# Kernel optimization log

Hardware: AMD Instinct MI355X
Metric: run time of the kernel (lower is better)

Reference implementation:

```python
import jax, jax.numpy as jnp
import numpy as np

B, S, D, H = 2, 2048, 1024, 16
DK = D // H
ROPE_BASE = 10000.0


def setup_inputs() -> dict:
    key = jax.random.key(0)
    ks = jax.random.split(key, 6)
    x = jax.random.normal(ks[0], (B, S, D), dtype=jnp.float32)
    # causal mask, broadcastable to [B,H,S,S]; masked_fill where mask==0
    mask = jnp.tril(jnp.ones((S, S), dtype=bool))[None, None]
    position_ids = jnp.tile(jnp.arange(S, dtype=jnp.int32)[None, :], (B, 1))
    sc = 1.0 / np.sqrt(D)
    Wq = jax.random.normal(ks[1], (D, D), dtype=jnp.float32) * sc
    Wk = jax.random.normal(ks[2], (D, D), dtype=jnp.float32) * sc
    Wv = jax.random.normal(ks[3], (D, D), dtype=jnp.float32) * sc
    Wo = jax.random.normal(ks[4], (D, D), dtype=jnp.float32) * sc
    bo = jnp.zeros((D,), dtype=jnp.float32)
    return {"x": x, "mask": mask, "position_ids": position_ids,
            "Wq": Wq, "Wk": Wk, "Wv": Wv, "Wo": Wo, "bo": bo}


def _rotate_half(t):
    t1, t2 = t[..., : t.shape[-1] // 2], t[..., t.shape[-1] // 2:]
    return jnp.concatenate((-t2, t1), axis=-1)


def reference(x, mask, position_ids, Wq, Wk, Wv, Wo, bo):
    b, s, d = x.shape
    h, dk = H, DK
    scale = 1.0 / np.sqrt(dk)

    def proj(W):  # torch Linear: x @ W.T -> [b,h,s,dk]
        return (x @ W.T).reshape(b, s, h, dk).transpose(0, 2, 1, 3)

    Q, K, V = proj(Wq), proj(Wk), proj(Wv)

    # rotary tables (computed in fp32, matching RotaryEmbedding)
    inv_freq = 1.0 / (ROPE_BASE ** (jnp.arange(0, dk, 2, dtype=jnp.float32) / dk))
    t = jnp.arange(s, dtype=jnp.float32)
    freqs = jnp.outer(t, inv_freq)            # [s, dk/2]
    emb = jnp.concatenate((freqs, freqs), -1) # [s, dk]
    cos = jnp.cos(emb)[position_ids][:, None]  # [b,1,s,dk]
    sin = jnp.sin(emb)[position_ids][:, None]
    Q = Q * cos + _rotate_half(Q) * sin
    K = K * cos + _rotate_half(K) * sin

    scores = jnp.einsum('bhqd,bhkd->bhqk', Q, K) * scale
    scores = jnp.where(mask, scores, jnp.float32(-1e9))
    attn = jax.nn.softmax(scores, axis=-1)  # dropout is identity in eval
    out = jnp.einsum('bhqk,bhkd->bhqd', attn, V)
    out = out.transpose(0, 2, 1, 3).reshape(b, s, d)
    return out @ Wo.T + bo
```

## Files before the change

### kernel.cpp

```cpp
#include <hip/hip_runtime.h>
#include <hip/hip_bf16.h>
#include <cstdint>

#define BB 2
#define SS 2048
#define DD 1024
#define HH 16
#define DK 64
#define MROWS (BB*SS)
#define NQKV  (3*DD)

typedef __bf16 bf16x8 __attribute__((ext_vector_type(8)));
typedef float  f32x4  __attribute__((ext_vector_type(4)));
typedef float  f32x16 __attribute__((ext_vector_type(16)));
typedef unsigned u32x2 __attribute__((ext_vector_type(2)));

static __device__ __forceinline__ unsigned short f2bf(float f) {
    __bf16 h = (__bf16)f;
    return __builtin_bit_cast(unsigned short, h);
}
static __device__ __forceinline__ float bf2f(unsigned short u) {
    return (float)__builtin_bit_cast(__bf16, u);
}

#define GLOAD16(gsrc, ldst) \
    __builtin_amdgcn_global_load_lds((const __attribute__((address_space(1))) void*)(gsrc), \
                                     (__attribute__((address_space(3))) void*)(ldst), 16, 0, 0)

static __device__ __forceinline__ void pl32_swap(unsigned &x, unsigned &y) {
#if __has_builtin(__builtin_amdgcn_permlane32_swap)
    u32x2 r = __builtin_amdgcn_permlane32_swap(x, y, false, false);
    x = r[0]; y = r[1];
#else
    asm volatile("v_permlane32_swap_b32 %0, %1" : "+v"(x), "+v"(y));
#endif
}
static __device__ __forceinline__ float swap_half(float v, bool hi) {
    unsigned x = __builtin_bit_cast(unsigned, v), y = x;
    pl32_swap(x, y);
    return __builtin_bit_cast(float, hi ? x : y);
}
template<int BASE> static __device__ __forceinline__ bf16x8 cvt_chunk(const f32x16 &p) {
    unsigned x0, y0, x1, y1;
    asm("v_cvt_pk_bf16_f32 %0, %1, %2" : "=v"(x0) : "v"(p[BASE+0]), "v"(p[BASE+1]));
    asm("v_cvt_pk_bf16_f32 %0, %1, %2" : "=v"(y0) : "v"(p[BASE+4]), "v"(p[BASE+5]));
    asm("v_cvt_pk_bf16_f32 %0, %1, %2" : "=v"(x1) : "v"(p[BASE+2]), "v"(p[BASE+3]));
    asm("v_cvt_pk_bf16_f32 %0, %1, %2" : "=v"(y1) : "v"(p[BASE+6]), "v"(p[BASE+7]));
    pl32_swap(x0, y0);
    pl32_swap(x1, y1);
    union { unsigned u[4]; bf16x8 v; } r;
    r.u[0] = x0; r.u[1] = x1; r.u[2] = y0; r.u[3] = y1;
    return r.v;
}

__global__ void cast_all(const float* __restrict__ x,  const float* __restrict__ wq,
                         const float* __restrict__ wk, const float* __restrict__ wv,
                         const float* __restrict__ wo,
                         unsigned short* __restrict__ xb, unsigned short* __restrict__ wqkv,
                         unsigned short* __restrict__ wob)
{
    const int NX = MROWS * DD;
    const int NW = DD * DD;
    const int total = (NX + 4 * NW) / 8;
    for (int i = blockIdx.x * blockDim.x + threadIdx.x; i < total; i += gridDim.x * blockDim.x) {
        int base = i * 8;
        const float* src; unsigned short* dst; int off;
        if      (base < NX)          { src = x;  dst = xb;          off = base; }
        else if (base < NX + NW)     { src = wq; dst = wqkv;        off = base - NX; }
        else if (base < NX + 2*NW)   { src = wk; dst = wqkv + NW;   off = base - NX - NW; }
        else if (base < NX + 3*NW)   { src = wv; dst = wqkv + 2*NW; off = base - NX - 2*NW; }
        else                         { src = wo; dst = wob;         off = base - NX - 3*NW; }
        float4 a = *(const float4*)(src + off);
        float4 b = *(const float4*)(src + off + 4);
        union { unsigned short s[8]; uint4 v; } u;
        u.s[0] = f2bf(a.x); u.s[1] = f2bf(a.y); u.s[2] = f2bf(a.z); u.s[3] = f2bf(a.w);
        u.s[4] = f2bf(b.x); u.s[5] = f2bf(b.y); u.s[6] = f2bf(b.z); u.s[7] = f2bf(b.w);
        *(uint4*)(dst + off) = u.v;
    }
}

__global__ void rope_table(float* __restrict__ tabc, float* __restrict__ tabs)
{
    int i = blockIdx.x * blockDim.x + threadIdx.x;
    int s = i >> 5, d = i & 31;
    float inv = exp2f(-(float)d * (13.287712379549449f / 32.f));
    float ang = (float)s * inv;
    tabc[i] = cosf(ang);
    tabs[i] = sinf(ang);
}

__global__ __launch_bounds__(256) void gemm_qkv(
    const unsigned short* __restrict__ A, const unsigned short* __restrict__ Bm,
    const int* __restrict__ pids,
    const float* __restrict__ tabc, const float* __restrict__ tabs,
    unsigned short* __restrict__ Qb, unsigned short* __restrict__ Kb,
    unsigned short* __restrict__ Vr)
{
    __shared__ __align__(16) unsigned short sA[128 * 64];
    __shared__ __align__(16) unsigned short sB[128 * 64];
    const int tid = threadIdx.x;
    const int w = tid >> 6, l = tid & 63;
    const int wm = w >> 1, wn = w & 1;
    const int lr = l & 15, lg = l >> 4;
    const int swz = (blockIdx.x & 7) * 96 + (blockIdx.x >> 3);
    const int bx = swz % 24, by = swz / 24;
    const int mBase = by * 128, nBase = bx * 128;
    const int srow = tid >> 3;
    const int skof = (tid & 7) * 8;

    f32x4 acc[4][4] = {};

    for (int kt = 0; kt < DD; kt += 64) {
        __syncthreads();
        #pragma unroll
        for (int i = 0; i < 4; ++i) {
            const unsigned short* srcA = A + (size_t)(mBase + i*32 + srow) * DD + kt + skof;
            GLOAD16(srcA, &sA[i*2048 + w*512]);
            const unsigned short* srcB = Bm + (size_t)(nBase + i*32 + srow) * DD + kt + skof;
            GLOAD16(srcB, &sB[i*2048 + w*512]);
        }
        __syncthreads();
        #pragma unroll
        for (int kk = 0; kk < 2; ++kk) {
            bf16x8 af[4], bfv[4];
            #pragma unroll
            for (int mi = 0; mi < 4; ++mi)
                af[mi] = *(const bf16x8*)&sA[(wm*64 + mi*16 + lr)*64 + kk*32 + lg*8];
            #pragma unroll
            for (int ni = 0; ni < 4; ++ni)
                bfv[ni] = *(const bf16x8*)&sB[(wn*64 + ni*16 + lr)*64 + kk*32 + lg*8];
            #pragma unroll
            for (int mi = 0; mi < 4; ++mi)
                #pragma unroll
                for (int ni = 0; ni < 4; ++ni)
                    acc[mi][ni] = __builtin_amdgcn_mfma_f32_16x16x32_bf16(af[mi], bfv[ni], acc[mi][ni], 0, 0, 0);
        }
    }

    if (bx < 16) {
        const bool isQ = bx < 8;
        unsigned short* dst = isQ ? Qb : Kb;
        const float qsc = isQ ? 0.1803368801111244f : 1.0f;
        const int colbase = (bx & 7)*128 + wn*64;
        #pragma unroll
        for (int mi = 0; mi < 4; ++mi) {
            #pragma unroll
            for (int j = 0; j < 4; ++j) {
                int row = mBase + wm*64 + mi*16 + lg*4 + j;
                int pos = pids[row];
                #pragma unroll
                for (int ni = 0; ni < 2; ++ni) {
                    int d = ni*16 + lr;
                    float cc = tabc[pos*32 + d];
                    float sn = tabs[pos*32 + d];
                    float a  = acc[mi][ni][j];
                    float bb = acc[mi][ni+2][j];
                    dst[(size_t)row * DD + colbase + d]      = f2bf((a*cc - bb*sn) * qsc);
                    dst[(size_t)row * DD + colbase + d + 32] = f2bf((bb*cc + a*sn) * qsc);
                }
            }
        }
    } else {
        const int colbase = (bx - 16)*128 + wn*64;
        #pragma unroll
        for (int mi = 0; mi < 4; ++mi) {
            #pragma unroll
            for (int j = 0; j < 4; ++j) {
                int row = mBase + wm*64 + mi*16 + lg*4 + j;
                #pragma unroll
                for (int ni = 0; ni < 4; ++ni)
                    Vr[(size_t)row * DD + colbase + ni*16 + lr] = f2bf(acc[mi][ni][j]);
            }
        }
    }
}

__global__ __launch_bounds__(256) void gemm_bt(
    const unsigned short* __restrict__ A, const unsigned short* __restrict__ Bm,
    float* __restrict__ Cout, const float* __restrict__ bias,
    int M, int N, int K)
{
    __shared__ __align__(16) unsigned short sA[2][128 * 64];
    __shared__ __align__(16) unsigned short sB[2][128 * 64];
    const int tid = threadIdx.x;
    const int w = tid >> 6, l = tid & 63;
    const int wm = w >> 1, wn = w & 1;
    const int lr = l & 15, lg = l >> 4;
    const int nwg = gridDim.x;
    const int cpx = nwg >> 3;
    const int swz = (blockIdx.x & 7) * cpx + (blockIdx.x >> 3);
    const int nbx = N >> 7;
    const int bx = swz % nbx, by = swz / nbx;
    const int mBase = by * 128, nBase = bx * 128;
    const int srow = tid >> 3;
    const int skof = (tid & 7) * 8;

    f32x4 acc[4][4] = {};

    #pragma unroll
    for (int i = 0; i < 4; ++i) {
        GLOAD16(A  + (size_t)(mBase + i*32 + srow) * K + skof, &sA[0][i*2048 + w*512]);
        GLOAD16(Bm + (size_t)(nBase + i*32 + srow) * K + skof, &sB[0][i*2048 + w*512]);
    }
    int cur = 0;

    for (int kt = 0; kt < K; kt += 64) {
        __syncthreads();
        if (kt + 64 < K) {
            #pragma unroll
            for (int i = 0; i < 4; ++i) {
                GLOAD16(A  + (size_t)(mBase + i*32 + srow) * K + kt + 64 + skof, &sA[cur^1][i*2048 + w*512]);
                GLOAD16(Bm + (size_t)(nBase + i*32 + srow) * K + kt + 64 + skof, &sB[cur^1][i*2048 + w*512]);
            }
        }
        #pragma unroll
        for (int kk = 0; kk < 2; ++kk) {
            bf16x8 af[4], bfv[4];
            #pragma unroll
            for (int mi = 0; mi < 4; ++mi)
                af[mi] = *(const bf16x8*)&sA[cur][(wm*64 + mi*16 + lr)*64 + kk*32 + lg*8];
            #pragma unroll
            for (int ni = 0; ni < 4; ++ni)
                bfv[ni] = *(const bf16x8*)&sB[cur][(wn*64 + ni*16 + lr)*64 + kk*32 + lg*8];
            #pragma unroll
            for (int mi = 0; mi < 4; ++mi)
                #pragma unroll
                for (int ni = 0; ni < 4; ++ni)
                    acc[mi][ni] = __builtin_amdgcn_mfma_f32_16x16x32_bf16(af[mi], bfv[ni], acc[mi][ni], 0, 0, 0);
        }
        cur ^= 1;
    }
    #pragma unroll
    for (int mi = 0; mi < 4; ++mi) {
        #pragma unroll
        for (int j = 0; j < 4; ++j) {
            int row = mBase + wm*64 + mi*16 + lg*4 + j;
            #pragma unroll
            for (int ni = 0; ni < 4; ++ni) {
                int col = nBase + wn*64 + ni*16 + lr;
                Cout[(size_t)row * N + col] = acc[mi][ni][j] + bias[col];
            }
        }
    }
}

__global__ __launch_bounds__(256) void v_transpose(
    const unsigned short* __restrict__ Vr, unsigned short* __restrict__ Vt)
{
    __shared__ __align__(16) unsigned short sT[64 * 64];
    const int bh = blockIdx.y;
    const int st = blockIdx.x;
    const int b = bh >> 4, h = bh & 15;
    const int tid = threadIdx.x;
    #pragma unroll
    for (int i = 0; i < 2; ++i) {
        int c = tid + i*256;
        int s = c >> 3, cb = c & 7;
        const unsigned short* src = Vr + (size_t)(b*SS + st*64 + s) * DD + h*64 + cb*8;
        uint4 v = *(const uint4*)src;
        *(uint4*)&sT[s*64 + ((cb ^ (s >> 3)) * 8)] = v;
    }
    __syncthreads();
    #pragma unroll
    for (int i = 0; i < 2; ++i) {
        int c = tid + i*256;
        int d = c >> 3, sb = c & 7;
        union { unsigned short u[8]; uint4 v; } o;
        #pragma unroll
        for (int e = 0; e < 8; ++e) {
            int s = sb*8 + e;
            o.u[e] = sT[s*64 + (((d >> 3) ^ (s >> 3)) * 8) + (d & 7)];
        }
        *(uint4*)(Vt + (size_t)(bh*64 + d) * SS + st*64 + sb*8) = o.v;
    }
}

__global__ __launch_bounds__(256, 2) void attn_fwd(
    const unsigned short* __restrict__ Qb,
    const unsigned short* __restrict__ Kb,
    const unsigned short* __restrict__ Vt,
    unsigned short* __restrict__ Ob)
{
    __shared__ __align__(16) unsigned short sK[2][64 * 64];
    __shared__ __align__(16) unsigned short sV[2][64 * 64];
    const int tid = threadIdx.x;
    const int w = tid >> 6, l = tid & 63;
    const int lq = l & 31;
    const int hi5 = l >> 5;
    const bool hb = hi5 != 0;

    const int xcd  = blockIdx.x & 7;
    const int c    = blockIdx.x >> 3;
    const int gsel = c & 3;
    const int t    = c >> 2;
    const int qt   = (t < 8) ? t : 23 - t;
    const int bh   = xcd * 4 + gsel;
    const int b = bh >> 4, h = bh & 15;

    const int srow = tid >> 3;
    const int skof = (tid & 7) * 8;
    const int sksw = skof ^ ((srow & 7) * 8);
    const int sw   = (lq & 7) * 8;
    const float THR = 12.0f;

    const unsigned kR0 = (unsigned)((b*SS + srow) * DD + h*64 + sksw);
    const unsigned kR1 = kR0 + (unsigned)(32 * DD);
    const unsigned vR0 = (unsigned)((bh*64 + srow) * SS + sksw);
    const unsigned vR1 = vR0 + (unsigned)(32 * SS);

    bf16x8 qf[4];
    {
        const unsigned short* qp = Qb + (size_t)(b*SS + qt*128 + w*32 + lq) * DD + h*64 + hi5*8;
        #pragma unroll
        for (int dkc = 0; dkc < 4; ++dkc)
            qf[dkc] = *(const bf16x8*)(qp + dkc*16);
    }
    const int q_lane = qt*128 + w*32 + lq;
    const int wbase  = qt*128 + w*32;
    const int total  = 2*qt + 2;

    f32x16 o0 = {}, o1 = {};
    float mrow = -3.0e38f, lsum = 0.f;
    int cur = 0;

    GLOAD16(Kb + kR0, &sK[0][w*512]);
    GLOAD16(Kb + kR1, &sK[0][2048 + w*512]);
    GLOAD16(Vt + vR0, &sV[0][w*512]);
    GLOAD16(Vt + vR1, &sV[0][2048 + w*512]);

    for (int kt = 0; kt < total; ++kt) {
        __syncthreads();
        if (kt + 1 < total) {
            unsigned ko = (unsigned)(kt + 1) << 16;
            unsigned vo = (unsigned)(kt + 1) << 6;
            GLOAD16(Kb + kR0 + ko, &sK[cur^1][w*512]);
            GLOAD16(Kb + kR1 + ko, &sK[cur^1][2048 + w*512]);
            GLOAD16(Vt + vR0 + vo, &sV[cur^1][w*512]);
            GLOAD16(Vt + vR1 + vo, &sV[cur^1][2048 + w*512]);
        }

        f32x16 p0 = {}, p1 = {};
        __builtin_amdgcn_s_setprio(1);
        #pragma unroll
        for (int dkc = 0; dkc < 4; ++dkc) {
            bf16x8 k0 = *(const bf16x8*)&sK[cur][lq*64 + ((dkc*16 + hi5*8) ^ sw)];
            p0 = __builtin_amdgcn_mfma_f32_32x32x16_bf16(k0, qf[dkc], p0, 0, 0, 0);
        }
        #pragma unroll
        for (int dkc = 0; dkc < 4; ++dkc) {
            bf16x8 k1 = *(const bf16x8*)&sK[cur][(32 + lq)*64 + ((dkc*16 + hi5*8) ^ sw)];
            p1 = __builtin_amdgcn_mfma_f32_32x32x16_bf16(k1, qf[dkc], p1, 0, 0, 0);
        }
        __builtin_amdgcn_s_setprio(0);

        if (kt*64 + 63 > wbase) {
            const int kb0 = kt*64 + 4*hi5;
            #pragma unroll
            for (int r = 0; r < 16; ++r) {
                const int cr = (r & 3) + 8*(r >> 2);
                if (kb0 + cr > q_lane)      p0[r] = -1e30f;
                if (kb0 + 32 + cr > q_lane) p1[r] = -1e30f;
            }
        }

        float tt[16];
        #pragma unroll
        for (int r = 0; r < 16; ++r) tt[r] = fmaxf(p0[r], p1[r]);
        #pragma unroll
        for (int s2 = 8; s2 >= 1; s2 >>= 1)
            #pragma unroll
            for (int r = 0; r < 8; ++r)
                if (r < s2) tt[r] = fmaxf(tt[r], tt[r + s2]);
        float tmx = fmaxf(tt[0], swap_half(tt[0], hb));

        float growth = tmx - mrow;
        if (!__all(growth <= THR)) {
            float mnew = fmaxf(mrow, tmx);
            float alpha = exp2f(mrow - mnew);
            lsum *= alpha;
            mrow = mnew;
            #pragma unroll
            for (int r = 0; r < 16; ++r) { o0[r] *= alpha; o1[r] *= alpha; }
        }

        #pragma unroll
        for (int r = 0; r < 16; ++r) {
            p0[r] = exp2f(p0[r] - mrow);
            p1[r] = exp2f(p1[r] - mrow);
        }
        float st[16];
        #pragma unroll
        for (int r = 0; r < 16; ++r) st[r] = p0[r] + p1[r];
        #pragma unroll
        for (int s2 = 8; s2 >= 1; s2 >>= 1)
            #pragma unroll
            for (int r = 0; r < 8; ++r)
                if (r < s2) st[r] += st[r + s2];
        lsum += st[0];

        __builtin_amdgcn_s_setprio(1);
        {
            bf16x8 pa, vf;
            pa = cvt_chunk<0>(p0);
            vf = *(const bf16x8*)&sV[cur][lq*64 + ((0*16 + hi5*8) ^ sw)];
            o0 = __builtin_amdgcn_mfma_f32_32x32x16_bf16(vf, pa, o0, 0, 0, 0);
            vf = *(const bf16x8*)&sV[cur][(32 + lq)*64 + ((0*16 + hi5*8) ^ sw)];
            o1 = __builtin_amdgcn_mfma_f32_32x32x16_bf16(vf, pa, o1, 0, 0, 0);
            pa = cvt_chunk<8>(p0);
            vf = *(const bf16x8*)&sV[cur][lq*64 + ((1*16 + hi5*8) ^ sw)];
            o0 = __builtin_amdgcn_mfma_f32_32x32x16_bf16(vf, pa, o0, 0, 0, 0);
            vf = *(const bf16x8*)&sV[cur][(32 + lq)*64 + ((1*16 + hi5*8) ^ sw)];
            o1 = __builtin_amdgcn_mfma_f32_32x32x16_bf16(vf, pa, o1, 0, 0, 0);
            pa = cvt_chunk<0>(p1);
            vf = *(const bf16x8*)&sV[cur][lq*64 + ((2*16 + hi5*8) ^ sw)];
            o0 = __builtin_amdgcn_mfma_f32_32x32x16_bf16(vf, pa, o0, 0, 0, 0);
            vf = *(const bf16x8*)&sV[cur][(32 + lq)*64 + ((2*16 + hi5*8) ^ sw)];
            o1 = __builtin_amdgcn_mfma_f32_32x32x16_bf16(vf, pa, o1, 0, 0, 0);
            pa = cvt_chunk<8>(p1);
            vf = *(const bf16x8*)&sV[cur][lq*64 + ((3*16 + hi5*8) ^ sw)];
            o0 = __builtin_amdgcn_mfma_f32_32x32x16_bf16(vf, pa, o0, 0, 0, 0);
            vf = *(const bf16x8*)&sV[cur][(32 + lq)*64 + ((3*16 + hi5*8) ^ sw)];
            o1 = __builtin_amdgcn_mfma_f32_32x32x16_bf16(vf, pa, o1, 0, 0, 0);
        }
        __builtin_amdgcn_s_setprio(0);
        cur ^= 1;
    }

    __syncthreads();
    float ls = lsum + swap_half(lsum, hb);
    float inv = 1.f / ls;
    unsigned short* sO = &sK[0][0] + w * 2048;

    #pragma unroll
    for (int g2 = 0; g2 < 4; ++g2) {
        unsigned ua, ub; uint2 t2;
        float v0 = o0[g2*4+0]*inv, v1 = o0[g2*4+1]*inv, v2 = o0[g2*4+2]*inv, v3 = o0[g2*4+3]*inv;
        asm("v_cvt_pk_bf16_f32 %0, %1, %2" : "=v"(ua) : "v"(v0), "v"(v1));
        asm("v_cvt_pk_bf16_f32 %0, %1, %2" : "=v"(ub) : "v"(v2), "v"(v3));
        t2.x = ua; t2.y = ub;
        *(uint2*)&sO[lq*64 + g2*8 + hi5*4] = t2;
        float w0 = o1[g2*4+0]*inv, w1 = o1[g2*4+1]*inv, w2 = o1[g2*4+2]*inv, w3 = o1[g2*4+3]*inv;
        asm("v_cvt_pk_bf16_f32 %0, %1, %2" : "=v"(ua) : "v"(w0), "v"(w1));
        asm("v_cvt_pk_bf16_f32 %0, %1, %2" : "=v"(ub) : "v"(w2), "v"(w3));
        t2.x = ua; t2.y = ub;
        *(uint2*)&sO[lq*64 + 32 + g2*8 + hi5*4] = t2;
    }
    asm volatile("s_waitcnt lgkmcnt(0)" ::: "memory");
    __builtin_amdgcn_sched_barrier(0);

    const int row = l >> 1, cb2 = (l & 1) * 32;
    const unsigned short* sOr = sO + row*64 + cb2;
    unsigned short* gp = Ob + (size_t)(b*SS + qt*128 + w*32 + row) * DD + h*64 + cb2;
    #pragma unroll
    for (int c2 = 0; c2 < 4; ++c2)
        *(uint4*)(gp + c2*8) = *(const uint4*)(sOr + c2*8);
}

extern "C" void kernel_launch(void* const* d_in, const int* in_sizes, int n_in,
                              void* d_out, int out_size, void* d_ws, size_t ws_size,
                              hipStream_t stream)
{
    const float* x  = (const float*)d_in[0];
    const int* pids = (const int*)d_in[2];
    const float* wq = (const float*)d_in[3];
    const float* wk = (const float*)d_in[4];
    const float* wv = (const float*)d_in[5];
    const float* wo = (const float*)d_in[6];
    const float* bo = (const float*)d_in[7];
    float* out = (float*)d_out;

    char* ws = (char*)d_ws;
    unsigned short* xb   = (unsigned short*)(ws);
    unsigned short* wqkv = (unsigned short*)(ws + (size_t)( 8u<<20));
    unsigned short* wob  = (unsigned short*)(ws + (size_t)(14u<<20));
    unsigned short* Vr   = (unsigned short*)(ws + (size_t)(16u<<20));
    unsigned short* Qb   = (unsigned short*)(ws + (size_t)(40u<<20));
    unsigned short* Kb   = (unsigned short*)(ws + (size_t)(48u<<20));
    unsigned short* Vt   = (unsigned short*)(ws + (size_t)(56u<<20));
    float* tabc          = (float*)(ws + (size_t)(64u<<20));
    float* tabs          = (float*)(ws + (size_t)(64u<<20) + (256u<<10));
    unsigned short* Ob   = xb;

    cast_all<<<dim3(4096), dim3(256), 0, stream>>>(x, wq, wk, wv, wo, xb, wqkv, wob);
    rope_table<<<dim3(256), dim3(256), 0, stream>>>(tabc, tabs);
    gemm_qkv<<<dim3(768), dim3(256), 0, stream>>>(
        xb, wqkv, pids, tabc, tabs, Qb, Kb, Vr);
    v_transpose<<<dim3(32, 32), dim3(256), 0, stream>>>(Vr, Vt);
    attn_fwd<<<dim3(512), dim3(256), 0, stream>>>(Qb, Kb, Vt, Ob);
    gemm_bt<<<dim3(256), dim3(256), 0, stream>>>(
        Ob, wob, out, bo, MROWS, DD, DD);
}
```

Baseline: 150.7 us.

## Enlarge QKV GEMM tiles to 256x256 with double-buffered swizzled LDS

Rewrites the fused QKV projection GEMM to use 256x256 output tiles with 512-thread blocks (8 waves), double-buffered shared memory staging, and an XOR swizzle on LDS columns to avoid bank conflicts. Global loads for the next K-slice are issued while MFMAs run on the current one, and s_setprio raises priority around the MFMA bursts. The goal is higher data reuse per byte loaded and overlap of loads with compute. In exchange the grid drops to 192 blocks, fewer than twice the CU count, so occupancy falls and tail effects may appear. Register pressure also rises with 32 accumulators per lane.

Result: faster. 138.6 us (-8.0%).

```diff
diff --git a/kernel.cpp b/kernel.cpp
--- a/kernel.cpp
+++ b/kernel.cpp
@@ -89,87 +89,107 @@
     tabs[i] = sinf(ang);
 }
 
-__global__ __launch_bounds__(256) void gemm_qkv(
+__global__ __launch_bounds__(512) void gemm_qkv(
     const unsigned short* __restrict__ A, const unsigned short* __restrict__ Bm,
     const int* __restrict__ pids,
     const float* __restrict__ tabc, const float* __restrict__ tabs,
     unsigned short* __restrict__ Qb, unsigned short* __restrict__ Kb,
     unsigned short* __restrict__ Vr)
 {
-    __shared__ __align__(16) unsigned short sA[128 * 64];
-    __shared__ __align__(16) unsigned short sB[128 * 64];
+    __shared__ __align__(16) unsigned short sA[2][16384];
+    __shared__ __align__(16) unsigned short sB[2][16384];
     const int tid = threadIdx.x;
     const int w = tid >> 6, l = tid & 63;
-    const int wm = w >> 1, wn = w & 1;
+    const int wm = w >> 2, wn = w & 3;
     const int lr = l & 15, lg = l >> 4;
-    const int swz = (blockIdx.x & 7) * 96 + (blockIdx.x >> 3);
-    const int bx = swz % 24, by = swz / 24;
-    const int mBase = by * 128, nBase = bx * 128;
-    const int srow = tid >> 3;
-    const int skof = (tid & 7) * 8;
-
-    f32x4 acc[4][4] = {};
-
-    for (int kt = 0; kt < DD; kt += 64) {
+    const int swz = (blockIdx.x & 7) * 24 + (blockIdx.x >> 3);
+    const int bx = swz % 12, by = swz / 12;
+    const int mBase = by * 256;
+    const int sr  = tid >> 3;
+    const int scb = (tid & 7) * 8;
+    const int sksw = scb ^ ((sr & 7) * 8);
+    const int rdsw = (lr & 7) * 8;
+
+    f32x4 acc[8][4] = {};
+
+    auto stage = [&](int kt, int bb) {
+        #pragma unroll
+        for (int r = 0; r < 4; ++r) {
+            GLOAD16(A  + (size_t)(mBase + r*64 + sr) * DD + kt + sksw,
+                    &sA[bb][r*4096 + sr*64 + scb]);
+            GLOAD16(Bm + (size_t)(bx*256 + r*64 + sr) * DD + kt + sksw,
+                    &sB[bb][r*4096 + sr*64 + scb]);
+        }
+    };
+
+    stage(0, 0);
+    __syncthreads();
+
+    for (int t = 0; t < 16; ++t) {
+        const int cur = t & 1;
+        if (t < 15) stage((t+1)*64, cur ^ 1);
+        #pragma unroll
+        for (int p = 0; p < 4; ++p) {
+            const int rh = p & 1, ks = p >> 1;
+            bf16x8 af[4], bfv[4];
+            #pragma unroll
+            for (int rf = 0; rf < 4; ++rf) {
+                int ra = wm*128 + rh*64 + rf*16 + lr;
+                af[rf] = *(const bf16x8*)&sA[cur][ra*64 + ((ks*32 + lg*8) ^ rdsw)];
+            }
+            #pragma unroll
+            for (int cf = 0; cf < 4; ++cf) {
+                int rb = wn*64 + cf*16 + lr;
+                bfv[cf] = *(const bf16x8*)&sB[cur][rb*64 + ((ks*32 + lg*8) ^ rdsw)];
+            }
+            asm volatile("s_waitcnt lgkmcnt(0)" ::: "memory");
+            __builtin_amdgcn_sched_barrier(0);
+            __builtin_amdgcn_s_setprio(1);
+            #pragma unroll
+            for (int rf = 0; rf < 4; ++rf)
+                #pragma unroll
+                for (int cf = 0; cf < 4; ++cf)
+                    acc[rh*4+rf][cf] = __builtin_amdgcn_mfma_f32_16x16x32_bf16(
+                        af[rf], bfv[cf], acc[rh*4+rf][cf], 0, 0, 0);
+            __builtin_amdgcn_s_setprio(0);
+            if (p < 3) __builtin_amdgcn_s_barrier();
+        }
         __syncthreads();
-        #pragma unroll
-        for (int i = 0; i < 4; ++i) {
-            const unsigned short* srcA = A + (size_t)(mBase + i*32 + srow) * DD + kt + skof;
-            GLOAD16(srcA, &sA[i*2048 + w*512]);
-            const unsigned short* srcB = Bm + (size_t)(nBase + i*32 + srow) * DD + kt + skof;
-            GLOAD16(srcB, &sB[i*2048 + w*512]);
-        }
-        __syncthreads();
-        #pragma unroll
-        for (int kk = 0; kk < 2; ++kk) {
-            bf16x8 af[4], bfv[4];
-            #pragma unroll
-            for (int mi = 0; mi < 4; ++mi)
-                af[mi] = *(const bf16x8*)&sA[(wm*64 + mi*16 + lr)*64 + kk*32 + lg*8];
-            #pragma unroll
-            for (int ni = 0; ni < 4; ++ni)
-                bfv[ni] = *(const bf16x8*)&sB[(wn*64 + ni*16 + lr)*64 + kk*32 + lg*8];
-            #pragma unroll
-            for (int mi = 0; mi < 4; ++mi)
-                #pragma unroll
-                for (int ni = 0; ni < 4; ++ni)
-                    acc[mi][ni] = __builtin_amdgcn_mfma_f32_16x16x32_bf16(af[mi], bfv[ni], acc[mi][ni], 0, 0, 0);
-        }
-    }
-
-    if (bx < 16) {
-        const bool isQ = bx < 8;
+    }
+
+    if (bx < 8) {
+        const bool isQ = bx < 4;
         unsigned short* dst = isQ ? Qb : Kb;
         const float qsc = isQ ? 0.1803368801111244f : 1.0f;
-        const int colbase = (bx & 7)*128 + wn*64;
-        #pragma unroll
-        for (int mi = 0; mi < 4; ++mi) {
+        const int colbase = (bx & 3)*256 + wn*64;
+        #pragma unroll
+        for (int rr = 0; rr < 8; ++rr) {
             #pragma unroll
             for (int j = 0; j < 4; ++j) {
-                int row = mBase + wm*64 + mi*16 + lg*4 + j;
+                int row = mBase + wm*128 + rr*16 + lg*4 + j;
                 int pos = pids[row];
                 #pragma unroll
-                for (int ni = 0; ni < 2; ++ni) {
-                    int d = ni*16 + lr;
+                for (int cf = 0; cf < 2; ++cf) {
+                    int d = cf*16 + lr;
                     float cc = tabc[pos*32 + d];
                     float sn = tabs[pos*32 + d];
-                    float a  = acc[mi][ni][j];
-                    float bb = acc[mi][ni+2][j];
-                    dst[(size_t)row * DD + colbase + d]      = f2bf((a*cc - bb*sn) * qsc);
-                    dst[(size_t)row * DD + colbase + d + 32] = f2bf((bb*cc + a*sn) * qsc);
+                    float a  = acc[rr][cf][j];
+                    float bb2 = acc[rr][cf+2][j];
+                    dst[(size_t)row * DD + colbase + d]      = f2bf((a*cc - bb2*sn) * qsc);
+                    dst[(size_t)row * DD + colbase + d + 32] = f2bf((bb2*cc + a*sn) * qsc);
                 }
             }
         }
     } else {
-        const int colbase = (bx - 16)*128 + wn*64;
-        #pragma unroll
-        for (int mi = 0; mi < 4; ++mi) {
+        const int colbase = (bx - 8)*256 + wn*64;
+        #pragma unroll
+        for (int rr = 0; rr < 8; ++rr) {
             #pragma unroll
             for (int j = 0; j < 4; ++j) {
-                int row = mBase + wm*64 + mi*16 + lg*4 + j;
+                int row = mBase + wm*128 + rr*16 + lg*4 + j;
                 #pragma unroll
-                for (int ni = 0; ni < 4; ++ni)
-                    Vr[(size_t)row * DD + colbase + ni*16 + lr] = f2bf(acc[mi][ni][j]);
+                for (int cf = 0; cf < 4; ++cf)
+                    Vr[(size_t)row * DD + colbase + cf*16 + lr] = f2bf(acc[rr][cf][j]);
             }
         }
     }
@@ -483,7 +503,7 @@
 
     cast_all<<<dim3(4096), dim3(256), 0, stream>>>(x, wq, wk, wv, wo, xb, wqkv, wob);
     rope_table<<<dim3(256), dim3(256), 0, stream>>>(tabc, tabs);
-    gemm_qkv<<<dim3(768), dim3(256), 0, stream>>>(
+    gemm_qkv<<<dim3(192), dim3(512), 0, stream>>>(
         xb, wqkv, pids, tabc, tabs, Qb, Kb, Vr);
     v_transpose<<<dim3(32, 32), dim3(256), 0, stream>>>(Vr, Vt);
     attn_fwd<<<dim3(512), dim3(256), 0, stream>>>(Qb, Kb, Vt, Ob);
```
